# Optimization experiments

Hardware: AMD Instinct MI355X
Metric: run time of the kernel (lower is better)

Reference implementation:

```python
import jax, jax.numpy as jnp
import numpy as np

HEADS = 8
DIM_HEAD = 64
SCALE = DIM_HEAD ** -0.5


def setup_inputs() -> dict:
    key = jax.random.key(0)
    ks = jax.random.split(key, 6)
    b, n, t, d, cond_dim, hidden = 2, 8, 1024, 512, 512, HEADS * DIM_HEAD
    return {
        "x": jax.random.normal(ks[0], (b * n, t, d), dtype=jnp.float32),
        "label_emb_mm": jax.random.normal(ks[1], (b, n, cond_dim), dtype=jnp.float32),
        "Wqkv": jax.random.normal(ks[2], (d, 3 * hidden), dtype=jnp.float32) * (d ** -0.5),
        "Wk": jax.random.normal(ks[3], (cond_dim, hidden), dtype=jnp.float32) * (cond_dim ** -0.5),
        "Wv": jax.random.normal(ks[4], (cond_dim, hidden), dtype=jnp.float32) * (cond_dim ** -0.5),
        "Wout": jax.random.normal(ks[5], (hidden, d), dtype=jnp.float32) * (hidden ** -0.5),
        "b": 2,
    }


def reference(x, label_emb_mm, Wqkv, Wk, Wv, Wout, b):
    bn, t, d = x.shape
    n = bn // b
    h, dh = HEADS, DIM_HEAD
    xb = x.reshape(b, n, t, d)
    # fused QKV projection: (b, n, t, 3*h*dh)
    qkv = xb @ Wqkv
    q, k, v = jnp.split(qkv, 3, axis=-1)

    def to_heads(z):  # (b, n, t, h*dh) -> (b, n, h, t, dh)
        return z.reshape(b, n, t, h, dh).transpose(0, 1, 3, 2, 4)

    q, k, v = to_heads(q), to_heads(k), to_heads(v)
    # per-frame conditioning K/V: one extra token per frame
    ek = (label_emb_mm @ Wk).reshape(b, n, 1, h, dh).transpose(0, 1, 3, 2, 4)
    ev = (label_emb_mm @ Wv).reshape(b, n, 1, h, dh).transpose(0, 1, 3, 2, 4)
    k = jnp.concatenate([ek, k], axis=-2)  # (b, n, h, 1+t, dh)
    v = jnp.concatenate([ev, v], axis=-2)
    q = q * SCALE
    sim = jnp.einsum("bnhid,bnhjd->bnhij", q, k)
    attn = jax.nn.softmax(sim, axis=-1)
    out = jnp.einsum("bnhij,bnhjd->bnhid", attn, v)
    out = out.transpose(0, 1, 3, 2, 4).reshape(b, n, t, h * dh)
    out = out @ Wout
    return out.reshape(b * n, t, d)
```

## Files before the change

kernel.cpp:

```cpp
#include <hip/hip_runtime.h>
#include <stdint.h>

typedef unsigned short u16;
typedef __bf16 bf16x8 __attribute__((ext_vector_type(8)));
typedef float f32x4 __attribute__((ext_vector_type(4)));
typedef float f32x16 __attribute__((ext_vector_type(16)));

__device__ __forceinline__ u16 f2bf(float f) {
  uint32_t u = __builtin_bit_cast(uint32_t, f);
  u += 0x7FFFu + ((u >> 16) & 1u);
  return (u16)(u >> 16);
}
__device__ __forceinline__ float bf2f(u16 v) {
  return __builtin_bit_cast(float, ((uint32_t)v) << 16);
}

#if __has_builtin(__builtin_amdgcn_exp2f)
__device__ __forceinline__ float exp2_fast(float x) { return __builtin_amdgcn_exp2f(x); }
#else
__device__ __forceinline__ float exp2_fast(float x) { return exp2f(x); }
#endif

__device__ __forceinline__ void gload_lds16(const u16* g, u16* l) {
  __builtin_amdgcn_global_load_lds(
      (const __attribute__((address_space(1))) uint32_t*)g,
      (__attribute__((address_space(3))) uint32_t*)l, 16, 0, 0);
}

__device__ __forceinline__ uint32_t cvtpk(float lo, float hi) {
  uint32_t r;
  asm("v_cvt_pk_bf16_f32 %0, %1, %2" : "=v"(r) : "v"(lo), "v"(hi));
  return r;
}
__device__ __forceinline__ void plswap(uint32_t& a, uint32_t& b) {
  asm volatile("v_permlane32_swap_b32 %0, %1" : "+v"(a), "+v"(b));
}

__global__ __launch_bounds__(256) void prep_kernel(
    const float* __restrict__ x, const float* __restrict__ Wqkv,
    const float* __restrict__ Wout, const float* __restrict__ label,
    const float* __restrict__ Wk, const float* __restrict__ Wv,
    u16* __restrict__ xb, u16* __restrict__ WqkvT, u16* __restrict__ WoutT,
    u16* __restrict__ ek, u16* __restrict__ ev, float qscale) {
  const int b = blockIdx.x;
  if (b < 4096) {
    int i = (b * 256 + threadIdx.x) * 8;
    float4 a = *(const float4*)(x + i);
    float4 c = *(const float4*)(x + i + 4);
    union { u16 u[8]; uint4 v; } r;
    r.u[0] = f2bf(a.x); r.u[1] = f2bf(a.y); r.u[2] = f2bf(a.z); r.u[3] = f2bf(a.w);
    r.u[4] = f2bf(c.x); r.u[5] = f2bf(c.y); r.u[6] = f2bf(c.z); r.u[7] = f2bf(c.w);
    *(uint4*)(xb + i) = r.v;
  } else if (b < 7168) {
    int id = (b - 4096) * 256 + threadIdx.x;
    int k = id & 511, nn = id >> 9;
    float v = Wqkv[(size_t)k * 1536 + nn];
    if (nn < 512) v *= qscale;
    WqkvT[id] = f2bf(v);
  } else if (b < 8192) {
    int id = (b - 7168) * 256 + threadIdx.x;
    int k = id & 511, nn = id >> 9;
    WoutT[id] = f2bf(Wout[(size_t)k * 512 + nn]);
  } else {
    int bb = b - 8192;
    int row = bb & 15;
    const float* W = (bb & 16) ? Wv : Wk;
    u16* o = (bb & 16) ? ev : ek;
    int c0 = threadIdx.x, c1 = threadIdx.x + 256;
    float a0 = 0.f, a1 = 0.f;
    for (int k = 0; k < 512; ++k) {
      float lv = label[row * 512 + k];
      const float* wr = W + (size_t)k * 512;
      a0 = fmaf(lv, wr[c0], a0);
      a1 = fmaf(lv, wr[c1], a1);
    }
    o[row * 512 + c0] = f2bf(a0);
    o[row * 512 + c1] = f2bf(a1);
  }
}

template <int MODE>
__global__ __launch_bounds__(512, 2) void gemm_bt_kernel(
    const u16* __restrict__ A, const u16* __restrict__ B,
    u16* __restrict__ OQ, u16* __restrict__ OKb, u16* __restrict__ OVT,
    float* __restrict__ OF, int K, int N) {
  __shared__ __align__(16) u16 As[2][128 * 64];
  __shared__ __align__(16) u16 Bs[2][256 * 64];
  const int tid = threadIdx.x;
  const int w = tid >> 6, lane = tid & 63;
  const int l15 = lane & 15, lg = lane >> 4;
  const int wr = w >> 2, wc = w & 3;

  constexpr int NBY = (MODE == 0) ? 6 : 2;
  const int q8 = gridDim.x >> 3;
  const int cf = blockIdx.x;
  const int wg = (cf & 7) * q8 + (cf >> 3);
  const int bx = wg / NBY, by = wg % NBY;

  const int srow = tid >> 3, schunk = tid & 7;
  const u16* Ag = A + (size_t)(bx * 128 + srow) * K + ((schunk ^ (srow & 7)) * 8);
  const u16* Bg = B + (size_t)(by * 256 + srow) * K + ((schunk ^ (srow & 7)) * 8);

  f32x4 acc[4][4] = {};

  const int nt = K >> 6;
#define STAGE(buf, k0)                                                     \
  {                                                                        \
    gload_lds16(Ag + (k0), &As[buf][(w * 8) * 64]);                        \
    gload_lds16(Ag + (k0) + (size_t)64 * K, &As[buf][(64 + w * 8) * 64]);  \
    _Pragma("unroll") for (int r = 0; r < 4; ++r)                          \
        gload_lds16(Bg + (k0) + (size_t)(r * 64) * K,                      \
                    &Bs[buf][(r * 64 + w * 8) * 64]);                      \
  }

  STAGE(0, 0);

  for (int t = 0; t < nt; ++t) {
    asm volatile("s_waitcnt vmcnt(0)" ::: "memory");
    __builtin_amdgcn_s_barrier();
    __builtin_amdgcn_sched_barrier(0);
    if (t + 1 < nt) STAGE((t + 1) & 1, (t + 1) * 64);

    const u16* Ab = &As[t & 1][0];
    const u16* Bb = &Bs[t & 1][0];
    bf16x8 a[4][2], b[4][2];
#pragma unroll
    for (int mi = 0; mi < 4; ++mi) {
      const int row = wr * 64 + mi * 16 + l15;
#pragma unroll
      for (int ks = 0; ks < 2; ++ks)
        a[mi][ks] = *(const bf16x8*)&Ab[row * 64 + (((ks * 4 + lg) ^ (row & 7)) * 8)];
    }
#pragma unroll
    for (int ni = 0; ni < 4; ++ni) {
      const int row = wc * 64 + ni * 16 + l15;
#pragma unroll
      for (int ks = 0; ks < 2; ++ks)
        b[ni][ks] = *(const bf16x8*)&Bb[row * 64 + (((ks * 4 + lg) ^ (row & 7)) * 8)];
    }
    __builtin_amdgcn_s_setprio(1);
#pragma unroll
    for (int ks = 0; ks < 2; ++ks)
#pragma unroll
      for (int mi = 0; mi < 4; ++mi)
#pragma unroll
        for (int ni = 0; ni < 4; ++ni)
          acc[mi][ni] = __builtin_amdgcn_mfma_f32_16x16x32_bf16(a[mi][ks], b[ni][ks], acc[mi][ni], 0, 0, 0);
    __builtin_amdgcn_s_setprio(0);
  }
#undef STAGE

  const int row0 = bx * 128 + wr * 64 + lg * 4;
  if constexpr (MODE == 1) {
#pragma unroll
    for (int mi = 0; mi < 4; ++mi)
#pragma unroll
      for (int ni = 0; ni < 4; ++ni) {
        int col = by * 256 + wc * 64 + ni * 16 + l15;
#pragma unroll
        for (int r = 0; r < 4; ++r)
          OF[(size_t)(row0 + mi * 16 + r) * N + col] = acc[mi][ni][r];
      }
  } else {
#pragma unroll
    for (int mi = 0; mi < 4; ++mi)
#pragma unroll
      for (int ni = 0; ni < 4; ++ni) {
        const int gcol = by * 256 + wc * 64 + ni * 16 + l15;
        const int sect = gcol >> 9;
        const int colL = gcol & 511;
        if (sect < 2) {
          u16* O = sect ? OKb : OQ;
#pragma unroll
          for (int r = 0; r < 4; ++r)
            O[(size_t)(row0 + mi * 16 + r) * 512 + colL] = f2bf(acc[mi][ni][r]);
        } else {
          int h = colL >> 6, dh = colL & 63;
          int rr = row0 + mi * 16;
          int bn = rr >> 10, t0 = rr & 1023;
          ushort4 pk;
          pk.x = f2bf(acc[mi][ni][0]);
          pk.y = f2bf(acc[mi][ni][1]);
          pk.z = f2bf(acc[mi][ni][2]);
          pk.w = f2bf(acc[mi][ni][3]);
          *(ushort4*)&OVT[(size_t)((bn * 8 + h) * 64 + dh) * 1024 + t0] = pk;
        }
      }
  }
}

__global__ __launch_bounds__(256, 2) void attn_kernel(
    const u16* __restrict__ Qb, const u16* __restrict__ Kb, const u16* __restrict__ VTb,
    const u16* __restrict__ ekb, const u16* __restrict__ evb, u16* __restrict__ Ob) {
  __shared__ __align__(16) u16 Kl[64 * 64];
  __shared__ __align__(16) u16 Vl[64 * 64];

  const int tid = threadIdx.x;
  const int w = tid >> 6, lane = tid & 63;
  const int l31 = lane & 31, hi = lane >> 5;
  const int lb = (blockIdx.x & 7) * 64 + (blockIdx.x >> 3);
  const int head = lb >> 2, qt = lb & 3;
  const int bn = head >> 3, h = head & 7;
  const int q0 = qt * 256 + w * 64;

  const int sr = tid >> 3, sj = tid & 7;
  const int sdst = (sj ^ (sr & 7)) * 8;
  const u16* KgA = Kb + (size_t)(bn * 1024 + sr) * 512 + h * 64 + sj * 8;
  const u16* VgA = VTb + (size_t)(head * 64 + sr) * 1024 + sj * 8;
  u16* KlD = &Kl[sr * 64 + sdst];
  u16* VlD = &Vl[sr * 64 + sdst];

  uint4 kp0, kp1, vp0, vp1;
  {
    kp0 = *(const uint4*)(KgA);
    kp1 = *(const uint4*)(KgA + (size_t)32 * 512);
    vp0 = *(const uint4*)(VgA);
    vp1 = *(const uint4*)(VgA + (size_t)32 * 1024);
  }

  bf16x8 qf[2][4];
#pragma unroll
  for (int qs = 0; qs < 2; ++qs)
#pragma unroll
    for (int c = 0; c < 4; ++c)
      qf[qs][c] = *(const bf16x8*)(Qb + (size_t)(bn * 1024 + q0 + qs * 32 + l31) * 512 +
                                   h * 64 + c * 16 + hi * 8);

  bf16x8 bones1;
  {
    union { u16 u[8]; bf16x8 v; } ob;
#pragma unroll
    for (int j = 0; j < 8; ++j) ob.u[j] = (u16)0x3F80;
    bones1 = ob.v;
  }

  f32x16 acc[2][2];
  f32x16 acc5[2];
  {
    float dot[2] = {0.f, 0.f};
#pragma unroll
    for (int c = 0; c < 4; ++c) {
      bf16x8 ekf = *(const bf16x8*)(ekb + bn * 512 + h * 64 + c * 16 + hi * 8);
#pragma unroll
      for (int qs = 0; qs < 2; ++qs)
#pragma unroll
        for (int j = 0; j < 8; ++j)
          dot[qs] += (float)qf[qs][c][j] * (float)ekf[j];
    }
    union { u16 u[8]; bf16x8 v; } pef[2], evf[2];
#pragma unroll
    for (int qs = 0; qs < 2; ++qs) {
      uint32_t a = __builtin_bit_cast(uint32_t, dot[qs]), b = a;
      plswap(a, b);
      float part = (lane < 32) ? __builtin_bit_cast(float, b) : __builtin_bit_cast(float, a);
      float pe = exp2_fast(dot[qs] + part);
#pragma unroll
      for (int j = 0; j < 8; ++j) pef[qs].u[j] = 0;
      if (hi == 0) pef[qs].u[0] = f2bf(pe);
    }
#pragma unroll
    for (int dt = 0; dt < 2; ++dt) {
#pragma unroll
      for (int j = 0; j < 8; ++j) evf[dt].u[j] = 0;
      if (hi == 0) evf[dt].u[0] = evb[bn * 512 + h * 64 + dt * 32 + l31];
    }
    f32x16 z = {};
#pragma unroll
    for (int qs = 0; qs < 2; ++qs) {
#pragma unroll
      for (int dt = 0; dt < 2; ++dt)
        acc[qs][dt] = __builtin_amdgcn_mfma_f32_32x32x16_bf16(pef[qs].v, evf[dt].v, z, 0, 0, 0);
      acc5[qs] = __builtin_amdgcn_mfma_f32_32x32x16_bf16(pef[qs].v, bones1, z, 0, 0, 0);
    }
  }

  for (int jt = 0; jt < 16; ++jt) {
    __syncthreads();
    *(uint4*)(KlD) = kp0;
    *(uint4*)(KlD + 32 * 64) = kp1;
    *(uint4*)(VlD) = vp0;
    *(uint4*)(VlD + 32 * 64) = vp1;
    __syncthreads();

    if (jt < 15) {
      const int j0 = (jt + 1) * 64;
      kp0 = *(const uint4*)(KgA + (size_t)j0 * 512);
      kp1 = *(const uint4*)(KgA + (size_t)(j0 + 32) * 512);
      vp0 = *(const uint4*)(VgA + j0);
      vp1 = *(const uint4*)(VgA + j0 + (size_t)32 * 1024);
    }

#pragma unroll
    for (int sub = 0; sub < 2; ++sub) {
      const int rk = sub * 32 + l31;
      bf16x8 kb[4];
#pragma unroll
      for (int c = 0; c < 4; ++c)
        kb[c] = *(const bf16x8*)&Kl[rk * 64 + (((c * 2 + hi) ^ (rk & 7)) * 8)];

      f32x16 s[2] = {};
#pragma unroll
      for (int qs = 0; qs < 2; ++qs)
#pragma unroll
        for (int c = 0; c < 4; ++c)
          s[qs] = __builtin_amdgcn_mfma_f32_32x32x16_bf16(kb[c], qf[qs][c], s[qs], 0, 0, 0);

      bf16x8 pa[2][2];
#pragma unroll
      for (int qs = 0; qs < 2; ++qs) {
        uint32_t wd[8];
#pragma unroll
        for (int i = 0; i < 8; ++i)
          wd[i] = cvtpk(exp2_fast(s[qs][2 * i]), exp2_fast(s[qs][2 * i + 1]));
        plswap(wd[0], wd[2]);
        plswap(wd[1], wd[3]);
        plswap(wd[4], wd[6]);
        plswap(wd[5], wd[7]);
        union { uint32_t w[4]; bf16x8 v; } f0, f1;
        f0.w[0] = wd[0]; f0.w[1] = wd[1]; f0.w[2] = wd[2]; f0.w[3] = wd[3];
        f1.w[0] = wd[4]; f1.w[1] = wd[5]; f1.w[2] = wd[6]; f1.w[3] = wd[7];
        pa[qs][0] = f0.v;
        pa[qs][1] = f1.v;
      }

#pragma unroll
      for (int dt = 0; dt < 2; ++dt) {
        const int rv = dt * 32 + l31;
#pragma unroll
        for (int ch = 0; ch < 2; ++ch) {
          bf16x8 vb = *(const bf16x8*)&Vl[rv * 64 + (((sub * 4 + ch * 2 + hi) ^ (rv & 7)) * 8)];
#pragma unroll
          for (int qs = 0; qs < 2; ++qs)
            acc[qs][dt] = __builtin_amdgcn_mfma_f32_32x32x16_bf16(pa[qs][ch], vb, acc[qs][dt], 0, 0, 0);
        }
      }
#pragma unroll
      for (int qs = 0; qs < 2; ++qs)
#pragma unroll
        for (int ch = 0; ch < 2; ++ch)
          acc5[qs] = __builtin_amdgcn_mfma_f32_32x32x16_bf16(pa[qs][ch], bones1, acc5[qs], 0, 0, 0);
    }
  }

#pragma unroll
  for (int qs = 0; qs < 2; ++qs)
#pragma unroll
    for (int r = 0; r < 16; ++r) {
      const float inv = 1.0f / acc5[qs][r];
      const int q = q0 + qs * 32 + (r & 3) + 8 * (r >> 2) + 4 * hi;
      u16* op = Ob + (size_t)(bn * 1024 + q) * 512 + h * 64 + l31;
      op[0] = f2bf(acc[qs][0][r] * inv);
      op[32] = f2bf(acc[qs][1][r] * inv);
    }
}

extern "C" void kernel_launch(void* const* d_in, const int* in_sizes, int n_in,
                              void* d_out, int out_size, void* d_ws, size_t ws_size,
                              hipStream_t stream) {
  (void)in_sizes; (void)n_in; (void)out_size; (void)ws_size;
  const float* x     = (const float*)d_in[0];
  const float* label = (const float*)d_in[1];
  const float* Wqkv  = (const float*)d_in[2];
  const float* Wk    = (const float*)d_in[3];
  const float* Wv    = (const float*)d_in[4];
  const float* Wout  = (const float*)d_in[5];
  float* out = (float*)d_out;

  char* ws = (char*)d_ws;
  u16* xb    = (u16*)(ws);
  u16* WqkvT = (u16*)(ws + 16777216);
  u16* WoutT = (u16*)(ws + 18350080);
  u16* ekb   = (u16*)(ws + 18874368);
  u16* evb   = (u16*)(ws + 18890752);
  u16* Qbuf  = (u16*)(ws + 18907136);
  u16* Kbuf  = (u16*)(ws + 35684352);
  u16* VTbuf = (u16*)(ws + 52461568);

  const float qscale = 0.125f * 1.4426950408889634f;

  prep_kernel<<<8224, 256, 0, stream>>>(x, Wqkv, Wout, label, Wk, Wv,
                                        xb, WqkvT, WoutT, ekb, evb, qscale);

  gemm_bt_kernel<0><<<768, 512, 0, stream>>>(xb, WqkvT, Qbuf, Kbuf, VTbuf, nullptr, 512, 1536);

  attn_kernel<<<512, 256, 0, stream>>>(Qbuf, Kbuf, VTbuf, ekb, evb, xb);

  gemm_bt_kernel<1><<<256, 512, 0, stream>>>(xb, WoutT, nullptr, nullptr, nullptr, out, 512, 512);
}
```

Before: 140.0 us.

## Triple-buffer GEMM LDS pipeline and parallelize label K/V projection with split-K

```diff
diff --git a/kernel.cpp b/kernel.cpp
--- a/kernel.cpp
+++ b/kernel.cpp
@@ -62,20 +62,26 @@
     int k = id & 511, nn = id >> 9;
     WoutT[id] = f2bf(Wout[(size_t)k * 512 + nn]);
   } else {
-    int bb = b - 8192;
-    int row = bb & 15;
-    const float* W = (bb & 16) ? Wv : Wk;
-    u16* o = (bb & 16) ? ev : ek;
-    int c0 = threadIdx.x, c1 = threadIdx.x + 256;
-    float a0 = 0.f, a1 = 0.f;
-    for (int k = 0; k < 512; ++k) {
-      float lv = label[row * 512 + k];
-      const float* wr = W + (size_t)k * 512;
-      a0 = fmaf(lv, wr[c0], a0);
-      a1 = fmaf(lv, wr[c1], a1);
-    }
-    o[row * 512 + c0] = f2bf(a0);
-    o[row * 512 + c1] = f2bf(a1);
+    __shared__ float sdata[256];
+    const int bb = b - 8192;
+    const int chunk = bb & 7, row = (bb >> 3) & 15;
+    const float* W = (bb & 128) ? Wv : Wk;
+    u16* o = (bb & 128) ? ev : ek;
+    const int tid = threadIdx.x;
+    const int col = chunk * 64 + (tid & 63);
+    const int ks = tid >> 6;
+    const float* lr = label + row * 512 + ks * 128;
+    const float* wp = W + (size_t)(ks * 128) * 512 + col;
+    float acc = 0.f;
+#pragma unroll 8
+    for (int i = 0; i < 128; ++i)
+      acc = fmaf(lr[i], wp[(size_t)i * 512], acc);
+    sdata[tid] = acc;
+    __syncthreads();
+    if (tid < 64) {
+      float t = sdata[tid] + sdata[tid + 64] + sdata[tid + 128] + sdata[tid + 192];
+      o[row * 512 + chunk * 64 + tid] = f2bf(t);
+    }
   }
 }
 
@@ -84,8 +90,8 @@
     const u16* __restrict__ A, const u16* __restrict__ B,
     u16* __restrict__ OQ, u16* __restrict__ OKb, u16* __restrict__ OVT,
     float* __restrict__ OF, int K, int N) {
-  __shared__ __align__(16) u16 As[2][128 * 64];
-  __shared__ __align__(16) u16 Bs[2][256 * 64];
+  __shared__ __align__(16) u16 As[3][128 * 64];
+  __shared__ __align__(16) u16 Bs[3][256 * 64];
   const int tid = threadIdx.x;
   const int w = tid >> 6, lane = tid & 63;
   const int l15 = lane & 15, lg = lane >> 4;
@@ -104,51 +110,57 @@
   f32x4 acc[4][4] = {};
 
   const int nt = K >> 6;
-#define STAGE(buf, k0)                                                     \
-  {                                                                        \
-    gload_lds16(Ag + (k0), &As[buf][(w * 8) * 64]);                        \
-    gload_lds16(Ag + (k0) + (size_t)64 * K, &As[buf][(64 + w * 8) * 64]);  \
-    _Pragma("unroll") for (int r = 0; r < 4; ++r)                          \
-        gload_lds16(Bg + (k0) + (size_t)(r * 64) * K,                      \
-                    &Bs[buf][(r * 64 + w * 8) * 64]);                      \
+#define STAGE(buf, k0)                                                      \
+  {                                                                         \
+    gload_lds16(Ag + (k0), &As[buf][(w * 8) * 64]);                         \
+    gload_lds16(Ag + (k0) + (size_t)64 * K, &As[buf][(64 + w * 8) * 64]);   \
+    _Pragma("unroll") for (int r = 0; r < 4; ++r)                           \
+        gload_lds16(Bg + (k0) + (size_t)(r * 64) * K,                       \
+                    &Bs[buf][(r * 64 + w * 8) * 64]);                       \
+  }
+#define COMPUTE(cb)                                                               \
+  {                                                                               \
+    const u16* Ab = &As[cb][0];                                                   \
+    const u16* Bb = &Bs[cb][0];                                                   \
+    bf16x8 a[4][2], b[4][2];                                                      \
+    _Pragma("unroll") for (int mi = 0; mi < 4; ++mi) {                            \
+      const int row = wr * 64 + mi * 16 + l15;                                    \
+      _Pragma("unroll") for (int ks = 0; ks < 2; ++ks)                            \
+          a[mi][ks] = *(const bf16x8*)&Ab[row * 64 + (((ks * 4 + lg) ^ (row & 7)) * 8)]; \
+    }                                                                             \
+    _Pragma("unroll") for (int ni = 0; ni < 4; ++ni) {                            \
+      const int row = wc * 64 + ni * 16 + l15;                                    \
+      _Pragma("unroll") for (int ks = 0; ks < 2; ++ks)                            \
+          b[ni][ks] = *(const bf16x8*)&Bb[row * 64 + (((ks * 4 + lg) ^ (row & 7)) * 8)]; \
+    }                                                                             \
+    __builtin_amdgcn_s_setprio(1);                                                \
+    _Pragma("unroll") for (int ks = 0; ks < 2; ++ks)                              \
+        _Pragma("unroll") for (int mi = 0; mi < 4; ++mi)                          \
+            _Pragma("unroll") for (int ni = 0; ni < 4; ++ni)                      \
+                acc[mi][ni] = __builtin_amdgcn_mfma_f32_16x16x32_bf16(             \
+                    a[mi][ks], b[ni][ks], acc[mi][ni], 0, 0, 0);                  \
+    __builtin_amdgcn_s_setprio(0);                                                \
   }
 
   STAGE(0, 0);
-
-  for (int t = 0; t < nt; ++t) {
-    asm volatile("s_waitcnt vmcnt(0)" ::: "memory");
+  STAGE(1, 64);
+
+  int cr = 0, cw = 2;
+  for (int t = 0; t < nt - 1; ++t) {
+    asm volatile("s_waitcnt vmcnt(6)" ::: "memory");
     __builtin_amdgcn_s_barrier();
     __builtin_amdgcn_sched_barrier(0);
-    if (t + 1 < nt) STAGE((t + 1) & 1, (t + 1) * 64);
-
-    const u16* Ab = &As[t & 1][0];
-    const u16* Bb = &Bs[t & 1][0];
-    bf16x8 a[4][2], b[4][2];
-#pragma unroll
-    for (int mi = 0; mi < 4; ++mi) {
-      const int row = wr * 64 + mi * 16 + l15;
-#pragma unroll
-      for (int ks = 0; ks < 2; ++ks)
-        a[mi][ks] = *(const bf16x8*)&Ab[row * 64 + (((ks * 4 + lg) ^ (row & 7)) * 8)];
-    }
-#pragma unroll
-    for (int ni = 0; ni < 4; ++ni) {
-      const int row = wc * 64 + ni * 16 + l15;
-#pragma unroll
-      for (int ks = 0; ks < 2; ++ks)
-        b[ni][ks] = *(const bf16x8*)&Bb[row * 64 + (((ks * 4 + lg) ^ (row & 7)) * 8)];
-    }
-    __builtin_amdgcn_s_setprio(1);
-#pragma unroll
-    for (int ks = 0; ks < 2; ++ks)
-#pragma unroll
-      for (int mi = 0; mi < 4; ++mi)
-#pragma unroll
-        for (int ni = 0; ni < 4; ++ni)
-          acc[mi][ni] = __builtin_amdgcn_mfma_f32_16x16x32_bf16(a[mi][ks], b[ni][ks], acc[mi][ni], 0, 0, 0);
-    __builtin_amdgcn_s_setprio(0);
-  }
+    if (t + 2 < nt) STAGE(cw, (t + 2) * 64);
+    COMPUTE(cr);
+    cr = (cr == 2) ? 0 : cr + 1;
+    cw = (cw == 2) ? 0 : cw + 1;
+  }
+  asm volatile("s_waitcnt vmcnt(0)" ::: "memory");
+  __builtin_amdgcn_s_barrier();
+  __builtin_amdgcn_sched_barrier(0);
+  COMPUTE(cr);
 #undef STAGE
+#undef COMPUTE
 
   const int row0 = bx * 128 + wr * 64 + lg * 4;
   if constexpr (MODE == 1) {
@@ -378,7 +390,7 @@
 
   const float qscale = 0.125f * 1.4426950408889634f;
 
-  prep_kernel<<<8224, 256, 0, stream>>>(x, Wqkv, Wout, label, Wk, Wv,
+  prep_kernel<<<8448, 256, 0, stream>>>(x, Wqkv, Wout, label, Wk, Wv,
                                         xb, WqkvT, WoutT, ekb, evb, qscale);
 
   gemm_bt_kernel<0><<<768, 512, 0, stream>>>(xb, WqkvT, Qbuf, Kbuf, VTbuf, nullptr, 512, 1536);
```

Result: faster. 122.4 us (-12.5%).
